# Kernel optimization log

Hardware: AMD Instinct MI355X
Metric: run time of the kernel (lower is better)

## Reference

```python
import jax, jax.numpy as jnp
import numpy as np

B = 16384      # batch
F = 39         # num fields
NUM = 13       # num numerical fields (len(mask_value[0]))
E = 64         # embed_dim
FD = 26000     # per-field vocab size
TOTAL_VOCAB = F * FD


def setup_inputs() -> dict:
    key = jax.random.key(0)
    k = jax.random.split(key, 7)
    features = jax.random.randint(k[0], (B, F), 0, FD)               # per-field ids
    mask = jax.random.randint(k[1], (B, NUM), 0, F)                  # field indices to rescale
    mask_apply = jax.random.randint(k[2], (B, NUM), 0, 2).astype(jnp.bool_)  # True where pd.isnull branch fires
    mask_value = jax.random.uniform(k[3], (B, NUM), dtype=jnp.float32)
    emb_table = jax.random.normal(k[4], (TOTAL_VOCAB, E), dtype=jnp.float32) * 0.01
    lin_w = jax.random.normal(k[5], (E,), dtype=jnp.float32) * 0.01  # FeaturesLinear: Linear(embed_dim, 1)
    lin_b = jnp.zeros((), dtype=jnp.float32)
    return {"features": features, "mask": mask, "mask_apply": mask_apply,
            "mask_value": mask_value, "emb_table": emb_table,
            "lin_w": lin_w, "lin_b": lin_b}


def reference(features, mask, mask_apply, mask_value, emb_table, lin_w, lin_b):
    # FeaturesEmbedding: add per-field offsets, then gather -> (B, F, E)
    offsets = (jnp.arange(F) * FD).astype(features.dtype)
    x = emb_table[features + offsets[None, :]]
    # masked per-row multiply: x[i, mask[i, j]] *= mask_value[i, j] where mask_apply
    scale = jnp.where(mask_apply, mask_value, jnp.float32(1.0))       # (B, NUM)
    bidx = jnp.arange(B)[:, None]                                     # (B, 1)
    x = x.at[bidx, mask].multiply(scale[..., None])                   # scatter-multiply, handles dup indices
    # FeaturesLinear: Linear(E, 1) per field, summed over fields -> (B,)
    logits = jnp.einsum('bfe,e->b', x, lin_w) + jnp.float32(F) * lin_b
    return jax.nn.sigmoid(logits)
```

## Files before the change

### kernel.cpp

```cpp
#include <hip/hip_runtime.h>
#include <hip/hip_bf16.h>

constexpr int Bn  = 16384;
constexpr int Fn  = 39;
constexpr int NUMn = 13;
constexpr int En  = 64;
constexpr int FDn = 26000;

__global__ __launch_bounds__(256) void fused_emb_logit(
    const int*   __restrict__ features,
    const int*   __restrict__ mask,
    const unsigned char* __restrict__ mask_apply,
    const float* __restrict__ mask_value,
    const float* __restrict__ emb,
    const float* __restrict__ lin_w,
    const float* __restrict__ lin_b,
    float*       __restrict__ out)
{
    const int lane = threadIdx.x & 63;
    const int row  = blockIdx.x * (blockDim.x >> 6) + (threadIdx.x >> 6);
    if (row >= Bn) return;

    const int s = lane & 15;
    const int g = lane >> 4;

    int   feat  = 0;
    float scale = 1.0f;
    if (lane < Fn) {
        feat = features[row * Fn + lane];
#pragma unroll
        for (int n = 0; n < NUMn; ++n) {
            const int   m  = mask[row * NUMn + n];
            const bool  ap = mask_apply[row * NUMn + n] != 0;
            const float mv = mask_value[row * NUMn + n];
            if (m == lane && ap) scale *= mv;
        }
    }

    float4 acc = make_float4(0.f, 0.f, 0.f, 0.f);
#pragma unroll
    for (int f0 = 0; f0 < Fn; f0 += 4) {
        const int f  = f0 + g;
        const int fc = (f < Fn) ? f : (Fn - 1);
        const int fi = __shfl(feat, fc, 64);
        const float scv = __shfl(scale, fc, 64);
        const float sc  = (f < Fn) ? scv : 0.0f;

        const int base = (fi + fc * FDn) * En + s * 4;
        const float4 v = *reinterpret_cast<const float4*>(emb + base);
        acc.x = fmaf(sc, v.x, acc.x);
        acc.y = fmaf(sc, v.y, acc.y);
        acc.z = fmaf(sc, v.z, acc.z);
        acc.w = fmaf(sc, v.w, acc.w);
    }

    const float4 w4 = *reinterpret_cast<const float4*>(lin_w + s * 4);
    float v = acc.x * w4.x + acc.y * w4.y + acc.z * w4.z + acc.w * w4.w;
#pragma unroll
    for (int off = 32; off > 0; off >>= 1)
        v += __shfl_down(v, off, 64);

    if (lane == 0) {
        const float logit = v + (float)Fn * lin_b[0];
        out[row] = 1.0f / (1.0f + expf(-logit));
    }
}

extern "C" void kernel_launch(void* const* d_in, const int* in_sizes, int n_in,
                              void* d_out, int out_size, void* d_ws, size_t ws_size,
                              hipStream_t stream) {
    const int*   features   = (const int*)  d_in[0];
    const int*   mask       = (const int*)  d_in[1];
    const unsigned char* mask_apply = (const unsigned char*)d_in[2];
    const float* mask_value = (const float*)d_in[3];
    const float* emb        = (const float*)d_in[4];
    const float* lin_w      = (const float*)d_in[5];
    const float* lin_b      = (const float*)d_in[6];
    float*       out        = (float*)d_out;

    const int threads = 256;
    const int blocks  = Bn / (threads / 64);
    fused_emb_logit<<<blocks, threads, 0, stream>>>(
        features, mask, mask_apply, mask_value, emb, lin_w, lin_b, out);
}
```

Baseline: 334.7 us.

## Precompute per-row table dot products with lin_w, then gather scalars

```diff
diff --git a/kernel.cpp b/kernel.cpp
--- a/kernel.cpp
+++ b/kernel.cpp
@@ -1,19 +1,62 @@
 #include <hip/hip_runtime.h>
 #include <hip/hip_bf16.h>
 
-constexpr int Bn  = 16384;
-constexpr int Fn  = 39;
+constexpr int Bn   = 16384;
+constexpr int Fn   = 39;
 constexpr int NUMn = 13;
-constexpr int En  = 64;
-constexpr int FDn = 26000;
+constexpr int En   = 64;
+constexpr int FDn  = 26000;
+constexpr int TV   = Fn * FDn;
 
-__global__ __launch_bounds__(256) void fused_emb_logit(
+__global__ __launch_bounds__(256) void dot_precompute(
+    const float* __restrict__ emb,
+    const float* __restrict__ lin_w,
+    float*       __restrict__ d)
+{
+    const int lane = threadIdx.x & 63;
+    const int wid  = (blockIdx.x * blockDim.x + threadIdx.x) >> 6;
+    const int s = lane & 15;
+    const int g = lane >> 4;
+
+    const float4 w4 = *reinterpret_cast<const float4*>(lin_w + s * 4);
+    const int row0 = wid * 16 + g;
+
+    if (row0 + 12 < TV) {
+#pragma unroll
+        for (int i = 0; i < 4; ++i) {
+            const int row = row0 + i * 4;
+            const float4 v = *reinterpret_cast<const float4*>(emb + row * En + s * 4);
+            float p = v.x * w4.x + v.y * w4.y + v.z * w4.z + v.w * w4.w;
+            p += __shfl_xor(p, 1, 64);
+            p += __shfl_xor(p, 2, 64);
+            p += __shfl_xor(p, 4, 64);
+            p += __shfl_xor(p, 8, 64);
+            if (s == 0) d[row] = p;
+        }
+    } else {
+#pragma unroll
+        for (int i = 0; i < 4; ++i) {
+            const int row = row0 + i * 4;
+            float p = 0.0f;
+            if (row < TV) {
+                const float4 v = *reinterpret_cast<const float4*>(emb + row * En + s * 4);
+                p = v.x * w4.x + v.y * w4.y + v.z * w4.z + v.w * w4.w;
+            }
+            p += __shfl_xor(p, 1, 64);
+            p += __shfl_xor(p, 2, 64);
+            p += __shfl_xor(p, 4, 64);
+            p += __shfl_xor(p, 8, 64);
+            if (s == 0 && row < TV) d[row] = p;
+        }
+    }
+}
+
+__global__ __launch_bounds__(256) void logits_kernel(
     const int*   __restrict__ features,
     const int*   __restrict__ mask,
     const unsigned char* __restrict__ mask_apply,
     const float* __restrict__ mask_value,
-    const float* __restrict__ emb,
-    const float* __restrict__ lin_w,
+    const float* __restrict__ d,
     const float* __restrict__ lin_b,
     float*       __restrict__ out)
 {
@@ -21,13 +64,11 @@
     const int row  = blockIdx.x * (blockDim.x >> 6) + (threadIdx.x >> 6);
     if (row >= Bn) return;
 
-    const int s = lane & 15;
-    const int g = lane >> 4;
-
-    int   feat  = 0;
-    float scale = 1.0f;
+    float v = 0.0f;
     if (lane < Fn) {
-        feat = features[row * Fn + lane];
+        const int feat = features[row * Fn + lane];
+        const float dv = d[feat + lane * FDn];
+        float scale = 1.0f;
 #pragma unroll
         for (int n = 0; n < NUMn; ++n) {
             const int   m  = mask[row * NUMn + n];
@@ -35,27 +76,8 @@
             const float mv = mask_value[row * NUMn + n];
             if (m == lane && ap) scale *= mv;
         }
+        v = scale * dv;
     }
-
-    float4 acc = make_float4(0.f, 0.f, 0.f, 0.f);
-#pragma unroll
-    for (int f0 = 0; f0 < Fn; f0 += 4) {
-        const int f  = f0 + g;
-        const int fc = (f < Fn) ? f : (Fn - 1);
-        const int fi = __shfl(feat, fc, 64);
-        const float scv = __shfl(scale, fc, 64);
-        const float sc  = (f < Fn) ? scv : 0.0f;
-
-        const int base = (fi + fc * FDn) * En + s * 4;
-        const float4 v = *reinterpret_cast<const float4*>(emb + base);
-        acc.x = fmaf(sc, v.x, acc.x);
-        acc.y = fmaf(sc, v.y, acc.y);
-        acc.z = fmaf(sc, v.z, acc.z);
-        acc.w = fmaf(sc, v.w, acc.w);
-    }
-
-    const float4 w4 = *reinterpret_cast<const float4*>(lin_w + s * 4);
-    float v = acc.x * w4.x + acc.y * w4.y + acc.z * w4.z + acc.w * w4.w;
 #pragma unroll
     for (int off = 32; off > 0; off >>= 1)
         v += __shfl_down(v, off, 64);
@@ -77,9 +99,12 @@
     const float* lin_w      = (const float*)d_in[5];
     const float* lin_b      = (const float*)d_in[6];
     float*       out        = (float*)d_out;
+    float*       d          = (float*)d_ws;
 
-    const int threads = 256;
-    const int blocks  = Bn / (threads / 64);
-    fused_emb_logit<<<blocks, threads, 0, stream>>>(
-        features, mask, mask_apply, mask_value, emb, lin_w, lin_b, out);
+    const int blocks1 = (TV + 63) / 64;
+    dot_precompute<<<blocks1, 256, 0, stream>>>(emb, lin_w, d);
+
+    const int blocks2 = Bn / 4;
+    logits_kernel<<<blocks2, 256, 0, stream>>>(
+        features, mask, mask_apply, mask_value, d, lin_b, out);
 }
```

Result: slower. 371.4 us (+11.0%).
